# Performance work log

Measured on AMD Instinct MI355X. Metric: run time of the kernel, lower is better.

Reference implementation:

```python
import jax, jax.numpy as jnp
import numpy as np

N_NODES = 50000
N_EDGES = 800000
NEG_SLOPE = 0.2


def gat_conv(x, src, dst, W, att_src, att_dst, bias, heads, out_ch, concat):
    """PyG-style GATConv (eval mode, self-loops already included in src/dst)."""
    N = x.shape[0]
    h = (x @ W).reshape(N, heads, out_ch)                      # [N,H,C]
    a_src = (h * att_src).sum(-1)                              # [N,H]
    a_dst = (h * att_dst).sum(-1)                              # [N,H]
    alpha = jax.nn.leaky_relu(a_src[src] + a_dst[dst], NEG_SLOPE)  # [E,H]
    # numerically stable segment softmax over incoming edges of each dst node
    amax = jax.ops.segment_max(alpha, dst, num_segments=N)     # [N,H]
    amax = jax.lax.stop_gradient(jnp.where(jnp.isfinite(amax), amax, 0.0))
    ex = jnp.exp(alpha - amax[dst])                            # [E,H]
    denom = jax.ops.segment_sum(ex, dst, num_segments=N)       # [N,H]
    coef = ex / (denom[dst] + 1e-16)                           # [E,H]
    msg = h[src] * coef[..., None]                             # [E,H,C]
    out = jax.ops.segment_sum(msg, dst, num_segments=N)        # [N,H,C]
    out = out.reshape(N, heads * out_ch) if concat else out.mean(axis=1)
    return out + bias


def setup_inputs() -> dict:
    key = jax.random.key(0)
    ks = jax.random.split(key, 12)
    x = jax.random.normal(ks[0], (N_NODES, 2), dtype=jnp.float32)
    edge_index = jax.random.randint(ks[1], (2, N_EDGES), 0, N_NODES, dtype=jnp.int64)
    # layer1: 2 -> 32, heads=4, concat
    W1 = jax.random.normal(ks[2], (2, 4 * 32), dtype=jnp.float32) * 0.5
    att_src1 = jax.random.normal(ks[3], (1, 4, 32), dtype=jnp.float32) * 0.1
    att_dst1 = jax.random.normal(ks[4], (1, 4, 32), dtype=jnp.float32) * 0.1
    b1 = jax.random.normal(ks[5], (128,), dtype=jnp.float32) * 0.01
    # layer2: 128 -> 128, heads=1, concat=False
    W2 = jax.random.normal(ks[6], (128, 128), dtype=jnp.float32) * (1.0 / np.sqrt(128.0))
    att_src2 = jax.random.normal(ks[7], (1, 1, 128), dtype=jnp.float32) * 0.1
    att_dst2 = jax.random.normal(ks[8], (1, 1, 128), dtype=jnp.float32) * 0.1
    b2 = jax.random.normal(ks[9], (128,), dtype=jnp.float32) * 0.01
    return {"x": x, "edge_index": edge_index, "W1": W1, "att_src1": att_src1,
            "att_dst1": att_dst1, "b1": b1, "W2": W2, "att_src2": att_src2,
            "att_dst2": att_dst2, "b2": b2}


def reference(x, edge_index, W1, att_src1, att_dst1, b1, W2, att_src2, att_dst2, b2):
    N = x.shape[0]
    loops = jnp.arange(N, dtype=edge_index.dtype)
    src = jnp.concatenate([edge_index[0], loops])  # PyG add_self_loops=True
    dst = jnp.concatenate([edge_index[1], loops])
    h = gat_conv(x, src, dst, W1, att_src1, att_dst1, b1, 4, 32, True)
    h = jax.nn.relu(h)
    h = gat_conv(h, src, dst, W2, att_src2, att_dst2, b2, 1, 128, False)
    # global_mean_pool with a single graph (batch all zeros) then squeeze(0)
    return h.mean(axis=0)  # [128]
```

## Files before the change

### kernel.cpp

```cpp
#include <hip/hip_runtime.h>

#define NN 50000
#define NE 800000
#define ET (NE + NN)
#define EPW 4096
#define NWGP ((ET + EPW - 1) / EPW)
#define NB 196
#define BCAP 6144

typedef unsigned short u16;
typedef unsigned int u32;
typedef unsigned char u8;

__device__ __forceinline__ float lrelu(float a) { return a > 0.f ? a : 0.2f * a; }

__global__ __launch_bounds__(256) void k_init(
        u32* __restrict__ bcur, u32* __restrict__ bcur2,
        u32* __restrict__ ovf, u32* __restrict__ ovf2,
        float* __restrict__ z, int* __restrict__ off, int* __restrict__ off_s,
        const float* __restrict__ W1, const float* __restrict__ as1,
        const float* __restrict__ ad1, const float* __restrict__ W2,
        const float* __restrict__ as2, const float* __restrict__ ad2,
        float* __restrict__ AD, float* __restrict__ vs, float* __restrict__ vd) {
    int i = threadIdx.x;
    bcur[i] = 0; bcur2[i] = 0;
    if (i == 0) { *ovf = 0; *ovf2 = 0; off[NN] = ET; off_s[NN] = ET; }
    if (i < 128) {
        z[i] = 0.f;
        float a = 0.f, d = 0.f;
        for (int c = 0; c < 128; ++c) {
            float wv = W2[i * 128 + c];
            a = fmaf(wv, as2[c], a);
            d = fmaf(wv, ad2[c], d);
        }
        vs[i] = a; vd[i] = d;
    }
    if (i >= 128 && i < 144) {
        int q = i - 128, isD = q >> 3, j = (q >> 2) & 1, hd = q & 3;
        const float* att = isD ? ad1 : as1;
        float acc = 0.f;
        for (int ch = 0; ch < 32; ++ch)
            acc = fmaf(W1[j * 128 + hd * 32 + ch], att[hd * 32 + ch], acc);
        AD[isD * 8 + j * 4 + hd] = acc;
    }
}

__global__ __launch_bounds__(256) void k_part(
        const int* __restrict__ ei,
        u32* __restrict__ bcur, u32* __restrict__ bcur2,
        u32* __restrict__ stg, u32* __restrict__ stg_s,
        u32* __restrict__ stg2, u32* __restrict__ stg2s,
        u32* __restrict__ ovf, u32* __restrict__ ovf2) {
    __shared__ u32 lcnt[256], sc[256], lbase[256], gbase[256];
    __shared__ u32 lpair[EPW];
    __shared__ u8  lbkt[EPW];
    int t = threadIdx.x;
    int e0 = blockIdx.x * EPW;

    u32 pr[16]; bool vd_[16]; u16 rk[16]; u8 bk[16];
#pragma unroll
    for (int j = 0; j < 16; ++j) {
        int e = e0 + j * 256 + t;
        vd_[j] = (e < ET);
        if (vd_[j]) {
            int s, d;
            if (e < NE) { s = ei[e]; d = ei[NE + e]; } else { s = d = e - NE; }
            pr[j] = ((u32)d << 16) | (u32)s;
        }
    }
    lcnt[t] = 0;
    __syncthreads();
#pragma unroll
    for (int j = 0; j < 16; ++j) if (vd_[j]) {
        int b = pr[j] >> 24;
        bk[j] = (u8)b;
        rk[j] = (u16)atomicAdd(&lcnt[b], 1u);
    }
    __syncthreads();
    u32 v = lcnt[t];
    sc[t] = v;
    __syncthreads();
#pragma unroll
    for (int st = 1; st < 256; st <<= 1) {
        u32 u = (t >= st) ? sc[t - st] : 0;
        __syncthreads();
        sc[t] += u;
        __syncthreads();
    }
    lbase[t] = sc[t] - v;
    gbase[t] = atomicAdd(&bcur[t], v);
    __syncthreads();
#pragma unroll
    for (int j = 0; j < 16; ++j) if (vd_[j]) {
        u32 idx = lbase[bk[j]] + rk[j];
        lpair[idx] = pr[j];
        lbkt[idx]  = bk[j];
    }
    __syncthreads();
    int nloc = lbase[255] + lcnt[255];
    for (int i = t; i < nloc; i += 256) {
        u32 b = lbkt[i];
        u32 g = gbase[b] + (i - lbase[b]);
        u32 p = lpair[i];
        if (g < BCAP) stg[(size_t)b * BCAP + g] = p;
        else { u32 o = atomicAdd(ovf, 1u); if (o < 4096) stg2[o] = p; }
    }
    __syncthreads();
    lcnt[t] = 0;
    __syncthreads();
#pragma unroll
    for (int j = 0; j < 16; ++j) if (vd_[j]) {
        int b = (pr[j] & 0xFFFFu) >> 8;
        bk[j] = (u8)b;
        rk[j] = (u16)atomicAdd(&lcnt[b], 1u);
    }
    __syncthreads();
    v = lcnt[t];
    sc[t] = v;
    __syncthreads();
#pragma unroll
    for (int st = 1; st < 256; st <<= 1) {
        u32 u = (t >= st) ? sc[t - st] : 0;
        __syncthreads();
        sc[t] += u;
        __syncthreads();
    }
    lbase[t] = sc[t] - v;
    gbase[t] = atomicAdd(&bcur2[t], v);
    __syncthreads();
#pragma unroll
    for (int j = 0; j < 16; ++j) if (vd_[j]) {
        u32 p2 = (pr[j] << 16) | (pr[j] >> 16);
        u32 idx = lbase[bk[j]] + rk[j];
        lpair[idx] = p2;
        lbkt[idx]  = bk[j];
    }
    __syncthreads();
    nloc = lbase[255] + lcnt[255];
    for (int i = t; i < nloc; i += 256) {
        u32 b = lbkt[i];
        u32 g = gbase[b] + (i - lbase[b]);
        u32 p = lpair[i];
        if (g < BCAP) stg_s[(size_t)b * BCAP + g] = p;
        else { u32 o = atomicAdd(ovf2, 1u); if (o < 4096) stg2s[o] = p; }
    }
}

__global__ __launch_bounds__(256) void k_place2(
        const u32* __restrict__ bcurA, const u32* __restrict__ bcurB,
        const u32* __restrict__ stgA, const u32* __restrict__ stgB,
        const u32* __restrict__ stg2A, const u32* __restrict__ stg2B,
        const u32* __restrict__ ovfA, const u32* __restrict__ ovfB,
        int* __restrict__ offA, int* __restrict__ offB,
        u16* __restrict__ outA, u16* __restrict__ outB) {
    __shared__ u32 sh[256], hist[256], sc[256], lcur[256];
    __shared__ u16 lcsr[BCAP];
    int blk = blockIdx.x, t = threadIdx.x;
    bool isB = (blk >= NB);
    int b = isB ? blk - NB : blk;
    const u32* bcur = isB ? bcurB : bcurA;
    const u32* stg  = isB ? stgB  : stgA;
    const u32* stg2 = isB ? stg2B : stg2A;
    const u32* ovf  = isB ? ovfB  : ovfA;
    int* off   = isB ? offB : offA;
    u16* out16 = isB ? outB : outA;

    u32 vv = (t < NB) ? bcur[t] : 0;
    sh[t] = vv;
    hist[t] = 0;
    __syncthreads();
#pragma unroll
    for (int s = 1; s < 256; s <<= 1) {
        u32 u = (t >= s) ? sh[t - s] : 0;
        __syncthreads();
        sh[t] += u;
        __syncthreads();
    }
    int S0 = (int)(sh[b] - bcur[b]);
    u32 cnt = bcur[b];
    u32 cmain = min(cnt, (u32)BCAP);

    for (u32 i = t; i < cmain; i += 256)
        atomicAdd(&hist[(stg[(size_t)b * BCAP + i] >> 16) & 255u], 1u);
    if (cnt > cmain) {
        u32 no = min(*ovf, 4096u);
        for (u32 i = t; i < no; i += 256) {
            u32 p = stg2[i];
            if ((p >> 24) == (u32)b) atomicAdd(&hist[(p >> 16) & 255u], 1u);
        }
    }
    __syncthreads();
    u32 v = hist[t];
    sc[t] = v;
    __syncthreads();
#pragma unroll
    for (int s = 1; s < 256; s <<= 1) {
        u32 u = (t >= s) ? sc[t - s] : 0;
        __syncthreads();
        sc[t] += u;
        __syncthreads();
    }
    u32 lexcl = sc[t] - v;
    int n = (b << 8) + t;
    if (n < NN) off[n] = S0 + (int)lexcl;
    lcur[t] = lexcl;
    __syncthreads();
    bool direct = (cnt > (u32)BCAP);
    for (u32 i = t; i < cmain; i += 256) {
        u32 p = stg[(size_t)b * BCAP + i];
        u32 r = atomicAdd(&lcur[(p >> 16) & 255u], 1u);
        if (direct) out16[S0 + r] = (u16)(p & 0xFFFFu);
        else        lcsr[r] = (u16)(p & 0xFFFFu);
    }
    if (cnt > cmain) {
        u32 no = min(*ovf, 4096u);
        for (u32 i = t; i < no; i += 256) {
            u32 p = stg2[i];
            if ((p >> 24) == (u32)b) {
                u32 r = atomicAdd(&lcur[(p >> 16) & 255u], 1u);
                if (direct) out16[S0 + r] = (u16)(p & 0xFFFFu);
                else        lcsr[r] = (u16)(p & 0xFFFFu);
            }
        }
    }
    __syncthreads();
    if (!direct)
        for (u32 i = t; i < cnt; i += 256) out16[S0 + i] = lcsr[i];
}

__global__ __launch_bounds__(128) void k_agg1x(
        const int* __restrict__ off, const u16* __restrict__ csr,
        const float* __restrict__ x, const float* __restrict__ AD,
        const float* __restrict__ W1, const float* __restrict__ b1,
        const float* __restrict__ vs, const float* __restrict__ vd,
        float* __restrict__ x2, float* __restrict__ asrc2,
        float* __restrict__ adst2) {
    int t = threadIdx.x;
    int wv = t >> 6, l = t & 63;
    int n = blockIdx.x * 2 + wv;
    if (n >= NN) return;
    int hd = l >> 4, li = l & 15;
    int e0 = off[n], deg = off[n + 1] - e0;
    float2 xd = *(const float2*)(x + 2 * n);
    float A0 = AD[hd], A1 = AD[4 + hd], D0 = AD[8 + hd], D1 = AD[12 + hd];
    float adn = fmaf(D0, xd.x, D1 * xd.y);

    float den = 0.f, S0 = 0.f, S1 = 0.f;
    for (int e = li; e < deg; e += 16) {
        int s = csr[e0 + e];
        float2 xv = *(const float2*)(x + 2 * s);
        float al = lrelu(fmaf(A0, xv.x, A1 * xv.y) + adn);
        float ex = __expf(fminf(al, 80.f));
        den += ex;
        S0 = fmaf(ex, xv.x, S0);
        S1 = fmaf(ex, xv.y, S1);
    }
#pragma unroll
    for (int m = 8; m >= 1; m >>= 1) {
        den += __shfl_xor(den, m);
        S0  += __shfl_xor(S0, m);
        S1  += __shfl_xor(S1, m);
    }
    float inv = 1.f / (den + 1e-16f);

    int c0 = 2 * l;
    float o0 = (S0 * W1[c0]     + S1 * W1[128 + c0])     * inv;
    float o1 = (S0 * W1[c0 + 1] + S1 * W1[128 + c0 + 1]) * inv;
    float v0 = fmaxf(o0 + b1[c0], 0.f);
    float v1 = fmaxf(o1 + b1[c0 + 1], 0.f);
    *(float2*)(x2 + (size_t)n * 128 + c0) = make_float2(v0, v1);

    float ps = fmaf(v0, vs[c0], v1 * vs[c0 + 1]);
    float pd = fmaf(v0, vd[c0], v1 * vd[c0 + 1]);
#pragma unroll
    for (int m = 32; m >= 1; m >>= 1) {
        ps += __shfl_xor(ps, m);
        pd += __shfl_xor(pd, m);
    }
    if (l == 0) { asrc2[n] = ps; adst2[n] = pd; }
}

__global__ __launch_bounds__(128) void k_den(
        const int* __restrict__ off, const u16* __restrict__ csr,
        const float* __restrict__ asrc2, const float* __restrict__ adst2,
        float* __restrict__ dinv) {
    int t = threadIdx.x;
    int g = t >> 4, li = t & 15;
    int n = blockIdx.x * 8 + g;
    if (n >= NN) return;
    int e0 = off[n], deg = off[n + 1] - e0;
    float adn = adst2[n];
    float den = 0.f;
    for (int e = li; e < deg; e += 16)
        den += __expf(fminf(lrelu(asrc2[csr[e0 + e]] + adn), 80.f));
#pragma unroll
    for (int m = 8; m >= 1; m >>= 1) den += __shfl_xor(den, m);
    if (li == 0) dinv[n] = 1.f / (den + 1e-16f);
}

__global__ __launch_bounds__(128) void k_wgath(
        const int* __restrict__ off_s, const u16* __restrict__ csc,
        const float* __restrict__ asrc2, const float* __restrict__ adst2,
        const float* __restrict__ dinv, float* __restrict__ w) {
    int t = threadIdx.x;
    int g = t >> 4, li = t & 15;
    int n = blockIdx.x * 8 + g;
    if (n >= NN) return;
    int e0 = off_s[n], deg = off_s[n + 1] - e0;
    float as = asrc2[n];
    float acc = 0.f;
    for (int e = li; e < deg; e += 16) {
        int d = csc[e0 + e];
        acc = fmaf(__expf(fminf(lrelu(as + adst2[d]), 80.f)), dinv[d], acc);
    }
#pragma unroll
    for (int m = 8; m >= 1; m >>= 1) acc += __shfl_xor(acc, m);
    if (li == 0) w[n] = acc;
}

__global__ __launch_bounds__(256) void k_wsum(const float* __restrict__ w,
                                              const float* __restrict__ x2,
                                              float* __restrict__ z) {
    __shared__ float red[256];
    int t = threadIdx.x, c = t & 127, rp = t >> 7;
    float acc = 0.f;
    for (int n = blockIdx.x * 2 + rp; n < NN; n += 2048)
        acc = fmaf(w[n], x2[(size_t)n * 128 + c], acc);
    red[t] = acc;
    __syncthreads();
    if (t < 128) atomicAdd(z + t, red[t] + red[t + 128]);
}

__global__ __launch_bounds__(128) void k_out(const float* __restrict__ z,
                                             const float* __restrict__ W2,
                                             const float* __restrict__ b2,
                                             float* __restrict__ out) {
    int c = threadIdx.x;
    float acc = 0.f;
    for (int k = 0; k < 128; ++k)
        acc = fmaf(z[k], W2[k * 128 + c], acc);
    out[c] = b2[c] + acc * (1.0f / NN);
}

extern "C" void kernel_launch(void* const* d_in, const int* in_sizes, int n_in,
                              void* d_out, int out_size, void* d_ws, size_t ws_size,
                              hipStream_t stream) {
    const float* x   = (const float*)d_in[0];
    const int*   ei  = (const int*)d_in[1];
    const float* W1  = (const float*)d_in[2];
    const float* as1 = (const float*)d_in[3];
    const float* ad1 = (const float*)d_in[4];
    const float* b1  = (const float*)d_in[5];
    const float* W2  = (const float*)d_in[6];
    const float* as2 = (const float*)d_in[7];
    const float* ad2 = (const float*)d_in[8];
    const float* b2  = (const float*)d_in[9];
    float* out = (float*)d_out;

    char* ws     = (char*)d_ws;
    float* x2    = (float*)ws;
    u32*  stg    = (u32*)x2;
    u32*  stg_s  = stg + (size_t)NB * BCAP;
    float* w     = x2 + (size_t)NN * 128;
    float* asrc2 = w + NN;
    float* adst2 = asrc2 + NN;
    float* dinv  = adst2 + NN;
    int* off     = (int*)(dinv + NN);
    int* off_s   = off + NN + 1;
    u32* bcur    = (u32*)(off_s + NN + 1);
    u32* bcur2   = bcur + 256;
    u32* ovf     = bcur2 + 256;
    u32* ovf2    = ovf + 4;
    u32* stg2    = ovf2 + 4;
    u32* stg2s   = stg2 + 4096;
    u16* csr16   = (u16*)(stg2s + 4096);
    u16* csc16   = csr16 + ET;
    float* AD    = (float*)(csc16 + ET);
    float* vs    = AD + 16;
    float* vd    = vs + 128;
    float* z     = vd + 128;

    k_init<<<1, 256, 0, stream>>>(bcur, bcur2, ovf, ovf2, z, off, off_s,
                                  W1, as1, ad1, W2, as2, ad2, AD, vs, vd);
    k_part<<<NWGP, 256, 0, stream>>>(ei, bcur, bcur2, stg, stg_s,
                                     stg2, stg2s, ovf, ovf2);
    k_place2<<<2 * NB, 256, 0, stream>>>(bcur, bcur2, stg, stg_s,
                                         stg2, stg2s, ovf, ovf2,
                                         off, off_s, csr16, csc16);
    k_agg1x<<<(NN + 1) / 2, 128, 0, stream>>>(off, csr16, x, AD, W1, b1,
                                              vs, vd, x2, asrc2, adst2);
    k_den<<<(NN + 7) / 8, 128, 0, stream>>>(off, csr16, asrc2, adst2, dinv);
    k_wgath<<<(NN + 7) / 8, 128, 0, stream>>>(off_s, csc16, asrc2, adst2, dinv, w);
    k_wsum<<<1024, 256, 0, stream>>>(w, x2, z);
    k_out<<<1, 128, 0, stream>>>(z, W2, b2, out);
}
```

Before: 130.6 us.

## Process all heads per 16-lane group in layer-1 aggregation and pack dst data

The layer-1 aggregation kernel now gives each node one 16-lane group that handles all four heads, where before each node had a full 64-lane wave with 16 lanes per head. Each neighbor's index and feature pair is now loaded once instead of four times, and W1, bias and the attention vectors are staged in shared memory before each lane writes 8 outputs with vector stores. Separately, the softmax denominator kernel writes the destination attention score and the inverse denominator together as a float2, so the weight-gather kernel does one random 8-byte load per edge instead of two 4-byte loads. The cost is four times more exp work per lane and more registers per thread.

```diff
diff --git a/kernel.cpp b/kernel.cpp
--- a/kernel.cpp
+++ b/kernel.cpp
@@ -235,55 +235,81 @@
         const float* __restrict__ vs, const float* __restrict__ vd,
         float* __restrict__ x2, float* __restrict__ asrc2,
         float* __restrict__ adst2) {
+    __shared__ float sW1[256], sb1[128], svs[128], svd[128];
     int t = threadIdx.x;
-    int wv = t >> 6, l = t & 63;
-    int n = blockIdx.x * 2 + wv;
+    if (t < 128) {
+        sW1[t] = W1[t]; sW1[128 + t] = W1[128 + t];
+        sb1[t] = b1[t]; svs[t] = vs[t]; svd[t] = vd[t];
+    }
+    __syncthreads();
+    int g = t >> 4, li = t & 15;
+    int n = blockIdx.x * 8 + g;
     if (n >= NN) return;
-    int hd = l >> 4, li = l & 15;
     int e0 = off[n], deg = off[n + 1] - e0;
     float2 xd = *(const float2*)(x + 2 * n);
-    float A0 = AD[hd], A1 = AD[4 + hd], D0 = AD[8 + hd], D1 = AD[12 + hd];
-    float adn = fmaf(D0, xd.x, D1 * xd.y);
-
-    float den = 0.f, S0 = 0.f, S1 = 0.f;
+    float A0[4], A1[4], adn[4];
+#pragma unroll
+    for (int h = 0; h < 4; ++h) {
+        A0[h] = AD[h]; A1[h] = AD[4 + h];
+        adn[h] = fmaf(AD[8 + h], xd.x, AD[12 + h] * xd.y);
+    }
+
+    float den[4] = {0.f, 0.f, 0.f, 0.f};
+    float S0[4] = {0.f, 0.f, 0.f, 0.f};
+    float S1[4] = {0.f, 0.f, 0.f, 0.f};
     for (int e = li; e < deg; e += 16) {
         int s = csr[e0 + e];
         float2 xv = *(const float2*)(x + 2 * s);
-        float al = lrelu(fmaf(A0, xv.x, A1 * xv.y) + adn);
-        float ex = __expf(fminf(al, 80.f));
-        den += ex;
-        S0 = fmaf(ex, xv.x, S0);
-        S1 = fmaf(ex, xv.y, S1);
+#pragma unroll
+        for (int h = 0; h < 4; ++h) {
+            float al = lrelu(fmaf(A0[h], xv.x, A1[h] * xv.y) + adn[h]);
+            float ex = __expf(fminf(al, 80.f));
+            den[h] += ex;
+            S0[h] = fmaf(ex, xv.x, S0[h]);
+            S1[h] = fmaf(ex, xv.y, S1[h]);
+        }
     }
 #pragma unroll
     for (int m = 8; m >= 1; m >>= 1) {
-        den += __shfl_xor(den, m);
-        S0  += __shfl_xor(S0, m);
-        S1  += __shfl_xor(S1, m);
-    }
-    float inv = 1.f / (den + 1e-16f);
-
-    int c0 = 2 * l;
-    float o0 = (S0 * W1[c0]     + S1 * W1[128 + c0])     * inv;
-    float o1 = (S0 * W1[c0 + 1] + S1 * W1[128 + c0 + 1]) * inv;
-    float v0 = fmaxf(o0 + b1[c0], 0.f);
-    float v1 = fmaxf(o1 + b1[c0 + 1], 0.f);
-    *(float2*)(x2 + (size_t)n * 128 + c0) = make_float2(v0, v1);
-
-    float ps = fmaf(v0, vs[c0], v1 * vs[c0 + 1]);
-    float pd = fmaf(v0, vd[c0], v1 * vd[c0 + 1]);
-#pragma unroll
-    for (int m = 32; m >= 1; m >>= 1) {
+#pragma unroll
+        for (int h = 0; h < 4; ++h) {
+            den[h] += __shfl_xor(den[h], m);
+            S0[h]  += __shfl_xor(S0[h], m);
+            S1[h]  += __shfl_xor(S1[h], m);
+        }
+    }
+    float inv[4];
+#pragma unroll
+    for (int h = 0; h < 4; ++h) inv[h] = 1.f / (den[h] + 1e-16f);
+
+    int hd = li >> 2;
+    float ov[8];
+    float ps = 0.f, pd = 0.f;
+#pragma unroll
+    for (int k = 0; k < 8; ++k) {
+        int c = li * 8 + k;
+        float o = (S0[hd] * sW1[c] + S1[hd] * sW1[128 + c]) * inv[hd];
+        float v = fmaxf(o + sb1[c], 0.f);
+        ov[k] = v;
+        ps = fmaf(v, svs[c], ps);
+        pd = fmaf(v, svd[c], pd);
+    }
+    *(float4*)(x2 + (size_t)n * 128 + li * 8) =
+        make_float4(ov[0], ov[1], ov[2], ov[3]);
+    *(float4*)(x2 + (size_t)n * 128 + li * 8 + 4) =
+        make_float4(ov[4], ov[5], ov[6], ov[7]);
+#pragma unroll
+    for (int m = 8; m >= 1; m >>= 1) {
         ps += __shfl_xor(ps, m);
         pd += __shfl_xor(pd, m);
     }
-    if (l == 0) { asrc2[n] = ps; adst2[n] = pd; }
+    if (li == 0) { asrc2[n] = ps; adst2[n] = pd; }
 }
 
 __global__ __launch_bounds__(128) void k_den(
         const int* __restrict__ off, const u16* __restrict__ csr,
         const float* __restrict__ asrc2, const float* __restrict__ adst2,
-        float* __restrict__ dinv) {
+        float2* __restrict__ dd) {
     int t = threadIdx.x;
     int g = t >> 4, li = t & 15;
     int n = blockIdx.x * 8 + g;
@@ -295,13 +321,13 @@
         den += __expf(fminf(lrelu(asrc2[csr[e0 + e]] + adn), 80.f));
 #pragma unroll
     for (int m = 8; m >= 1; m >>= 1) den += __shfl_xor(den, m);
-    if (li == 0) dinv[n] = 1.f / (den + 1e-16f);
+    if (li == 0) dd[n] = make_float2(adn, 1.f / (den + 1e-16f));
 }
 
 __global__ __launch_bounds__(128) void k_wgath(
         const int* __restrict__ off_s, const u16* __restrict__ csc,
-        const float* __restrict__ asrc2, const float* __restrict__ adst2,
-        const float* __restrict__ dinv, float* __restrict__ w) {
+        const float* __restrict__ asrc2, const float2* __restrict__ dd,
+        float* __restrict__ w) {
     int t = threadIdx.x;
     int g = t >> 4, li = t & 15;
     int n = blockIdx.x * 8 + g;
@@ -310,8 +336,8 @@
     float as = asrc2[n];
     float acc = 0.f;
     for (int e = li; e < deg; e += 16) {
-        int d = csc[e0 + e];
-        acc = fmaf(__expf(fminf(lrelu(as + adst2[d]), 80.f)), dinv[d], acc);
+        float2 di = dd[csc[e0 + e]];
+        acc = fmaf(__expf(fminf(lrelu(as + di.x), 80.f)), di.y, acc);
     }
 #pragma unroll
     for (int m = 8; m >= 1; m >>= 1) acc += __shfl_xor(acc, m);
@@ -364,8 +390,8 @@
     float* w     = x2 + (size_t)NN * 128;
     float* asrc2 = w + NN;
     float* adst2 = asrc2 + NN;
-    float* dinv  = adst2 + NN;
-    int* off     = (int*)(dinv + NN);
+    float2* dd   = (float2*)(adst2 + NN);
+    int* off     = (int*)(dd + NN);
     int* off_s   = off + NN + 1;
     u32* bcur    = (u32*)(off_s + NN + 1);
     u32* bcur2   = bcur + 256;
@@ -387,10 +413,10 @@
     k_place2<<<2 * NB, 256, 0, stream>>>(bcur, bcur2, stg, stg_s,
                                          stg2, stg2s, ovf, ovf2,
                                          off, off_s, csr16, csc16);
-    k_agg1x<<<(NN + 1) / 2, 128, 0, stream>>>(off, csr16, x, AD, W1, b1,
+    k_agg1x<<<(NN + 7) / 8, 128, 0, stream>>>(off, csr16, x, AD, W1, b1,
                                               vs, vd, x2, asrc2, adst2);
-    k_den<<<(NN + 7) / 8, 128, 0, stream>>>(off, csr16, asrc2, adst2, dinv);
-    k_wgath<<<(NN + 7) / 8, 128, 0, stream>>>(off_s, csc16, asrc2, adst2, dinv, w);
+    k_den<<<(NN + 7) / 8, 128, 0, stream>>>(off, csr16, asrc2, adst2, dd);
+    k_wgath<<<(NN + 7) / 8, 128, 0, stream>>>(off_s, csc16, asrc2, dd, w);
     k_wsum<<<1024, 256, 0, stream>>>(w, x2, z);
     k_out<<<1, 128, 0, stream>>>(z, W2, b2, out);
 }
```

Measured after the change: 123.5 us (median of 2 runs). -5.4%, faster.
